# Kernel optimization log

Hardware: AMD Instinct MI355X
Metric: run time of the kernel (lower is better)

## Reference

```python
import jax, jax.numpy as jnp
import numpy as np

N, E, D, H = 50000, 1600000, 256, 256
EPS = 1e-5

def prelu(x, a):
    return jnp.where(x >= 0, x, a * x)

def batch_norm(x, gamma, beta):
    # training-mode BatchNorm1d: stats over the node (batch) dim
    mu = jnp.mean(x, axis=0)
    var = jnp.var(x, axis=0)
    return (x - mu) * jax.lax.rsqrt(var + EPS) * gamma + beta

def gcn_conv(x, edge_index, W, b):
    # PyG GCNConv: h = XW, add self-loops, symmetric norm, scatter-add, + bias
    h = x @ W
    n = x.shape[0]
    row = jnp.concatenate([edge_index[0], jnp.arange(n)])
    col = jnp.concatenate([edge_index[1], jnp.arange(n)])
    w = jnp.ones(row.shape[0], dtype=x.dtype)
    deg = jax.ops.segment_sum(w, col, num_segments=n)
    dinv = jnp.where(deg > 0, jax.lax.rsqrt(deg), 0.0)
    norm = dinv[row] * w * dinv[col]  # [E+N]
    msg = h[row] * norm[:, None]      # [E+N, H] gathered messages
    out = jax.ops.segment_sum(msg, col, num_segments=n)
    return out + b

def setup_inputs() -> dict:
    key = jax.random.key(0)
    ks = jax.random.split(key, 10)
    x = jax.random.normal(ks[0], (N, D), dtype=jnp.float32)
    edge_index = jax.random.randint(ks[1], (2, E), 0, N).astype(jnp.int64)
    s1 = 1.0 / np.sqrt(D)
    s2 = 1.0 / np.sqrt(H)
    return {
        "x": x,
        "edge_index": edge_index,
        "W1": jax.random.uniform(ks[2], (D, H), jnp.float32, -s1, s1),
        "b1": jnp.zeros((H,), jnp.float32),
        "W2": jax.random.uniform(ks[3], (H, H), jnp.float32, -s2, s2),
        "b2": jnp.zeros((H,), jnp.float32),
        "prelu_a": jnp.asarray(0.25, jnp.float32),
        "bn_gamma": jnp.ones((H,), jnp.float32),
        "bn_beta": jnp.zeros((H,), jnp.float32),
        "proj_W": jax.random.uniform(ks[4], (H, H), jnp.float32, -s2, s2),
        "proj_b": jnp.zeros((H,), jnp.float32),
        "pbn_gamma": jnp.ones((H,), jnp.float32),
        "pbn_beta": jnp.zeros((H,), jnp.float32),
        "prelu2_a": jnp.asarray(0.25, jnp.float32),
    }

def reference(x, edge_index, W1, b1, W2, b2, prelu_a, bn_gamma, bn_beta,
              proj_W, proj_b, pbn_gamma, pbn_beta, prelu2_a):
    # eval-mode dropout (identity); BN uses batch stats
    z = prelu(gcn_conv(x, edge_index, W1, b1), prelu_a)
    z = prelu(gcn_conv(z, edge_index, W2, b2), prelu_a)
    z = batch_norm(z, bn_gamma, bn_beta)
    p = prelu(batch_norm(z @ proj_W + proj_b, pbn_gamma, pbn_beta), prelu2_a)
    return (z, p)
```

## Files before the change

### kernel.cpp

```cpp
#include <hip/hip_runtime.h>
#include <hip/hip_bf16.h>


#define CAP 96
#define NPB 64
#define CHUNK 2048
#define SEGBIG 2432
#define MAXBKT 1024
#define SEGSTR 16

typedef __attribute__((ext_vector_type(8))) short short8;
typedef __attribute__((ext_vector_type(4))) float f32x4;

__device__ __forceinline__ float bf2f(unsigned short u) {
    union { unsigned int i; float f; } v; v.i = ((unsigned int)u) << 16; return v.f;
}
__device__ __forceinline__ unsigned short f2bf(float f) {
    __hip_bfloat16 h = __float2bfloat16(f);
    return *reinterpret_cast<unsigned short*>(&h);
}

__global__ __launch_bounds__(256) void k_zero(int* segcnt, int nbkt, float* stats) {
    int i = blockIdx.x * 256 + threadIdx.x;
    if (i < nbkt * SEGSTR) segcnt[i] = 0;
    if (i < 2048) stats[i] = 0.0f;
}

__global__ __launch_bounds__(64) void k_zrow(unsigned short* hs, int N) {
    ((ushort4*)hs)[(size_t)N * 64 + threadIdx.x] = ushort4{0, 0, 0, 0};
}

__global__ __launch_bounds__(256) void k_binh(const int* __restrict__ row, const int* __restrict__ col,
                                              unsigned* __restrict__ bins, int* __restrict__ segcnt,
                                              int E, int nbkt) {
    __shared__ int hist[MAXBKT];
    __shared__ int base[MAXBKT];
    int e0 = blockIdx.x * CHUNK;
    int eend = e0 + CHUNK; if (eend > E) eend = E;
    for (int b = threadIdx.x; b < nbkt; b += 256) hist[b] = 0;
    __syncthreads();
    for (int e = e0 + threadIdx.x; e < eend; e += 256)
        atomicAdd(&hist[col[e] >> 6], 1);
    __syncthreads();
    for (int b = threadIdx.x; b < nbkt; b += 256) {
        int h = hist[b];
        base[b] = h ? atomicAdd(&segcnt[b * SEGSTR], h) : 0;
        hist[b] = 0;
    }
    __syncthreads();
    for (int e = e0 + threadIdx.x; e < eend; e += 256) {
        int v = col[e], r = row[e];
        int b = v >> 6;
        int p = base[b] + atomicAdd(&hist[b], 1);
        if (p < SEGBIG) bins[(size_t)b * SEGBIG + p] = ((unsigned)r << 6) | (unsigned)(v & (NPB - 1));
    }
}

__global__ __launch_bounds__(256) void k_csr(const unsigned* __restrict__ bins, const int* __restrict__ segcnt,
                                             int* __restrict__ csr, int* __restrict__ fillp,
                                             float* __restrict__ dinv, int N) {
    __shared__ int cnt[NPB];
    int bkt = blockIdx.x;
    if (threadIdx.x < NPB) cnt[threadIdx.x] = 0;
    __syncthreads();
    int m = segcnt[bkt * SEGSTR]; if (m > SEGBIG) m = SEGBIG;
    const unsigned* b = bins + (size_t)bkt * SEGBIG;
    for (int i = threadIdx.x; i < m; i += 256) {
        unsigned ent = b[i];
        int loc = (int)(ent & (NPB - 1));
        int r   = (int)(ent >> 6);
        int p = atomicAdd(&cnt[loc], 1);
        if (p < CAP) csr[(size_t)(bkt * NPB + loc) * CAP + p] = r;
    }
    __syncthreads();
    if (threadIdx.x < NPB) {
        int v = bkt * NPB + threadIdx.x;
        if (v < N) {
            int c = cnt[threadIdx.x];
            int real = c < CAP ? c : CAP;
            int pc = (real + 15) & ~15;
            if (pc > CAP) pc = CAP;
            int* lst = csr + (size_t)v * CAP;
            for (int p = real; p < pc; ++p) lst[p] = N;
            fillp[v] = pc;
            dinv[v] = rsqrtf(1.0f + (float)c);
        }
    }
}

__global__ __launch_bounds__(256) void k_castx(const float* __restrict__ x, unsigned short* __restrict__ xb, size_t n4) {
    size_t stride = (size_t)gridDim.x * blockDim.x;
    for (size_t i = (size_t)blockIdx.x * blockDim.x + threadIdx.x; i < n4; i += stride) {
        float4 v = ((const float4*)x)[i];
        ushort4 o; o.x = f2bf(v.x); o.y = f2bf(v.y); o.z = f2bf(v.z); o.w = f2bf(v.w);
        ((ushort4*)xb)[i] = o;
    }
}

__global__ __launch_bounds__(256) void k_wt(const float* __restrict__ W, unsigned short* __restrict__ Wt,
                                            const float* __restrict__ scp) {
    __shared__ float t[32][33];
    int bx = blockIdx.x * 32, by = blockIdx.y * 32;
    int x = threadIdx.x & 31, y = threadIdx.x >> 5;
#pragma unroll
    for (int i = 0; i < 32; i += 8) {
        float s = scp ? scp[by + y + i] : 1.0f;
        t[y + i][x] = W[(size_t)(by + y + i) * 256 + bx + x] * s;
    }
    __syncthreads();
#pragma unroll
    for (int i = 0; i < 32; i += 8)
        Wt[(size_t)(bx + y + i) * 256 + by + x] = f2bf(t[x][y + i]);
}

__global__ __launch_bounds__(256) void k_tvec(const float* __restrict__ W, const float* __restrict__ sh,
                                              float* __restrict__ tvec) {
    int n = threadIdx.x;
    float s = 0.0f;
    for (int k = 0; k < 256; ++k) s += sh[k] * W[(size_t)k * 256 + n];
    tvec[n] = s;
}

__global__ __launch_bounds__(256) void k_gemm_bf16(const unsigned short* __restrict__ A,
                                                   const unsigned short* __restrict__ Bt,
                                                   unsigned short* __restrict__ C,
                                                   const float* __restrict__ dinv, int use_scale,
                                                   const float* __restrict__ tvec, int use_bias,
                                                   int M) {
    __shared__ unsigned short buf[16384];
    unsigned short* As = buf;
    unsigned short* Bs = buf + 8192;
    int tid  = threadIdx.x;
    int lane = tid & 63, wid = tid >> 6;
    int wr = wid >> 1, wc = wid & 1;
    int row0 = blockIdx.x * 128;
    int col0 = blockIdx.y * 128;

    f32x4 acc[4][4];
#pragma unroll
    for (int m = 0; m < 4; ++m)
#pragma unroll
        for (int n = 0; n < 4; ++n) acc[m][n] = f32x4{0.f, 0.f, 0.f, 0.f};

    int srow = lane >> 3;
    int sk   = (lane & 7) * 8;

    for (int k0 = 0; k0 < 256; k0 += 64) {
#pragma unroll
        for (int i = 0; i < 4; ++i) {
            int u = i * 4 + wid;
            int arow = row0 + u * 8 + srow;
            if (arow >= M) arow = M - 1;
            const unsigned short* ga = A  + (size_t)arow * 256 + k0 + sk;
            const unsigned short* gb = Bt + (size_t)(col0 + u * 8 + srow) * 256 + k0 + sk;
            __builtin_amdgcn_global_load_lds((const __attribute__((address_space(1))) void*)ga,
                (__attribute__((address_space(3))) void*)(As + u * 512), 16, 0, 0);
            __builtin_amdgcn_global_load_lds((const __attribute__((address_space(1))) void*)gb,
                (__attribute__((address_space(3))) void*)(Bs + u * 512), 16, 0, 0);
        }
        __syncthreads();
#pragma unroll
        for (int kk = 0; kk < 64; kk += 32) {
            short8 a[4], b[4];
#pragma unroll
            for (int m = 0; m < 4; ++m)
                a[m] = *(const short8*)(As + (wr * 64 + m * 16 + (lane & 15)) * 64 + kk + (lane >> 4) * 8);
#pragma unroll
            for (int n = 0; n < 4; ++n)
                b[n] = *(const short8*)(Bs + (wc * 64 + n * 16 + (lane & 15)) * 64 + kk + (lane >> 4) * 8);
#pragma unroll
            for (int m = 0; m < 4; ++m)
#pragma unroll
                for (int n = 0; n < 4; ++n)
                    acc[m][n] = __builtin_amdgcn_mfma_f32_16x16x32_bf16(a[m], b[n], acc[m][n], 0, 0, 0);
        }
        __syncthreads();
    }

    float tn[4] = {0.f, 0.f, 0.f, 0.f};
    if (use_bias) {
#pragma unroll
        for (int n = 0; n < 4; ++n) tn[n] = tvec[col0 + wc * 64 + n * 16 + (lane & 15)];
    }
#pragma unroll
    for (int m = 0; m < 4; ++m)
#pragma unroll
        for (int r = 0; r < 4; ++r) {
            int lr = wr * 64 + m * 16 + (lane >> 4) * 4 + r;
#pragma unroll
            for (int n = 0; n < 4; ++n)
                buf[lr * 128 + wc * 64 + n * 16 + (lane & 15)] = f2bf(acc[m][n][r] + tn[n]);
        }
    __syncthreads();
#pragma unroll
    for (int j = 0; j < 8; ++j) {
        int c = j * 256 + tid;
        int r = c >> 4, cc = c & 15;
        int grow = row0 + r;
        if (grow < M) {
            short8 v = *(const short8*)(buf + r * 128 + cc * 8);
            if (use_scale) {
                float d = dinv[grow];
                short8 o;
#pragma unroll
                for (int t = 0; t < 8; ++t)
                    o[t] = (short)f2bf(bf2f((unsigned short)v[t]) * d);
                v = o;
            }
            *(short8*)(C + (size_t)grow * 256 + col0 + cc * 8) = v;
        }
    }
}

__global__ __launch_bounds__(256) void k_agg_bf(const unsigned short* __restrict__ hs,
                                                unsigned short* __restrict__ outb,
                                                const float* __restrict__ dinv, const int* __restrict__ csr,
                                                const int* __restrict__ fillp, const float* __restrict__ bias,
                                                const float* __restrict__ aptr, int N) {
    int wv = threadIdx.x >> 6, lane = threadIdx.x & 63;
    int v = blockIdx.x * 4 + wv;
    if (v >= N) return;
    const ushort4* h4 = (const ushort4*)hs;
    float dv = dinv[v];
    ushort4 hv = h4[(size_t)v * 64 + lane];
    float s0 = bf2f(hv.x), s1 = bf2f(hv.y), s2 = bf2f(hv.z), s3 = bf2f(hv.w);
    int n = fillp[v];
    const int* lst = csr + (size_t)v * CAP;
    for (int i = 0; i < n; i += 16) {
        int u[16];
        ushort4 a[16];
#pragma unroll
        for (int t = 0; t < 16; ++t) u[t] = lst[i + t];
#pragma unroll
        for (int t = 0; t < 16; ++t) a[t] = h4[(size_t)u[t] * 64 + lane];
#pragma unroll
        for (int t = 0; t < 16; ++t) {
            s0 += bf2f(a[t].x); s1 += bf2f(a[t].y);
            s2 += bf2f(a[t].z); s3 += bf2f(a[t].w);
        }
    }
    float al = *aptr;
    float4 bb = *(const float4*)(bias + lane * 4);
    float o0 = dv * s0 + bb.x, o1 = dv * s1 + bb.y, o2 = dv * s2 + bb.z, o3 = dv * s3 + bb.w;
    o0 = o0 >= 0.f ? o0 : al * o0;
    o1 = o1 >= 0.f ? o1 : al * o1;
    o2 = o2 >= 0.f ? o2 : al * o2;
    o3 = o3 >= 0.f ? o3 : al * o3;
    ushort4 o; o.x = f2bf(o0); o.y = f2bf(o1); o.z = f2bf(o2); o.w = f2bf(o3);
    ((ushort4*)outb)[(size_t)v * 64 + lane] = o;
}

__global__ __launch_bounds__(256) void k_bnstats_v(const unsigned short* __restrict__ X, float* __restrict__ sums, int N) {
    int w = threadIdx.x >> 6, lane = threadIdx.x & 63;
    int c4 = lane * 4;
    float4 s = {0.f, 0.f, 0.f, 0.f}, q = {0.f, 0.f, 0.f, 0.f};
    int rstride = gridDim.x * 4;
    for (int r = blockIdx.x * 4 + w; r < N; r += rstride) {
        ushort4 x4 = ((const ushort4*)X)[(size_t)r * 64 + lane];
        float a = bf2f(x4.x), b = bf2f(x4.y), c = bf2f(x4.z), d = bf2f(x4.w);
        s.x += a; s.y += b; s.z += c; s.w += d;
        q.x += a * a; q.y += b * b; q.z += c * c; q.w += d * d;
    }
    atomicAdd(&sums[c4 + 0], s.x); atomicAdd(&sums[c4 + 1], s.y);
    atomicAdd(&sums[c4 + 2], s.z); atomicAdd(&sums[c4 + 3], s.w);
    atomicAdd(&sums[256 + c4 + 0], q.x); atomicAdd(&sums[256 + c4 + 1], q.y);
    atomicAdd(&sums[256 + c4 + 2], q.z); atomicAdd(&sums[256 + c4 + 3], q.w);
}

__global__ __launch_bounds__(256) void k_bnfinal(float* stats, const float* __restrict__ gamma,
                                                 const float* __restrict__ beta, float invN) {
    int c = threadIdx.x;
    float mu = stats[c] * invN;
    float var = stats[256 + c] * invN - mu * mu;
    float rstd = rsqrtf(var + 1e-5f);
    float sc = rstd * gamma[c];
    stats[512 + c] = sc;
    stats[768 + c] = beta[c] - mu * sc;
}

__global__ __launch_bounds__(256) void k_bnapply_z(const unsigned short* __restrict__ in,
                                                   float* __restrict__ zout,
                                                   const float* __restrict__ scale, const float* __restrict__ shift,
                                                   size_t n4) {
    size_t stride = (size_t)gridDim.x * blockDim.x;
    for (size_t i = (size_t)blockIdx.x * blockDim.x + threadIdx.x; i < n4; i += stride) {
        int c4 = (int)(i & 63) * 4;
        ushort4 x4 = ((const ushort4*)in)[i];
        float4 sc = *(const float4*)(scale + c4);
        float4 sh = *(const float4*)(shift + c4);
        float4 y;
        y.x = bf2f(x4.x) * sc.x + sh.x;
        y.y = bf2f(x4.y) * sc.y + sh.y;
        y.z = bf2f(x4.z) * sc.z + sh.z;
        y.w = bf2f(x4.w) * sc.w + sh.w;
        ((float4*)zout)[i] = y;
    }
}

__global__ __launch_bounds__(256) void k_bnapply_p(const unsigned short* __restrict__ in,
                                                   float* __restrict__ pout,
                                                   const float* __restrict__ scale, const float* __restrict__ shift,
                                                   const float* __restrict__ aptr, size_t n4) {
    size_t stride = (size_t)gridDim.x * blockDim.x;
    float a = *aptr;
    for (size_t i = (size_t)blockIdx.x * blockDim.x + threadIdx.x; i < n4; i += stride) {
        int c4 = (int)(i & 63) * 4;
        ushort4 x4 = ((const ushort4*)in)[i];
        float4 sc = *(const float4*)(scale + c4);
        float4 sh = *(const float4*)(shift + c4);
        float4 y;
        y.x = bf2f(x4.x) * sc.x + sh.x;
        y.y = bf2f(x4.y) * sc.y + sh.y;
        y.z = bf2f(x4.z) * sc.z + sh.z;
        y.w = bf2f(x4.w) * sc.w + sh.w;
        y.x = y.x >= 0.f ? y.x : a * y.x;
        y.y = y.y >= 0.f ? y.y : a * y.y;
        y.z = y.z >= 0.f ? y.z : a * y.z;
        y.w = y.w >= 0.f ? y.w : a * y.w;
        ((float4*)pout)[i] = y;
    }
}

extern "C" void kernel_launch(void* const* d_in, const int* in_sizes, int n_in,
                              void* d_out, int out_size, void* d_ws, size_t ws_size,
                              hipStream_t stream) {
    const float* x     = (const float*)d_in[0];
    const int*   ei    = (const int*)d_in[1];
    const float* W1    = (const float*)d_in[2];
    const float* b1    = (const float*)d_in[3];
    const float* W2    = (const float*)d_in[4];
    const float* b2    = (const float*)d_in[5];
    const float* aptr  = (const float*)d_in[6];
    const float* gamma = (const float*)d_in[7];
    const float* beta  = (const float*)d_in[8];
    const float* projW = (const float*)d_in[9];
    const float* pgamma = (const float*)d_in[11];
    const float* pbeta  = (const float*)d_in[12];
    const float* a2ptr  = (const float*)d_in[13];

    int N = in_sizes[0] / 256;
    int E = in_sizes[1] / 2;
    const int* row = ei;
    const int* col = ei + E;

    float* out  = (float*)d_out;
    float* zout = out;
    float* pout = out + (size_t)N * 256;

    int nbkt = (N + NPB - 1) / NPB;

    size_t rowsz = (size_t)(N + 1) * 256;
    unsigned short* B0 = (unsigned short*)d_ws;
    unsigned short* B1 = B0 + rowsz;
    unsigned short* B2 = B1 + rowsz;
    unsigned short* Wt = B2 + rowsz;
    float* dinv  = (float*)(Wt + 3 * 65536);
    int*   fillp = (int*)(dinv + N + 1);
    int*   csr   = fillp + N;
    float* stats = (float*)(csr + (size_t)N * CAP);
    float* tvec  = stats + 2048;
    int*   segcnt= (int*)(tvec + 256);
    unsigned* bins = (unsigned*)(segcnt + (size_t)nbkt * SEGSTR);

    int nb_binh = (E + CHUNK - 1) / CHUNK;
    dim3 ggrid((N + 127) / 128, 2);
    dim3 wgrid(8, 8);
    int  agrid = (N + 3) / 4;
    size_t n4 = (size_t)N * 64;

    k_zero <<<64, 256, 0, stream>>>(segcnt, nbkt, stats);
    k_zrow <<<1, 64, 0, stream>>>(B1, N);
    k_binh <<<nb_binh, 256, 0, stream>>>(row, col, bins, segcnt, E, nbkt);
    k_csr  <<<nbkt, 256, 0, stream>>>(bins, segcnt, csr, fillp, dinv, N);
    k_castx<<<2048, 256, 0, stream>>>(x, B0, n4);
    k_wt   <<<wgrid, 256, 0, stream>>>(W1, Wt,         nullptr);
    k_wt   <<<wgrid, 256, 0, stream>>>(W2, Wt + 65536, nullptr);

    k_gemm_bf16<<<ggrid, 256, 0, stream>>>(B0, Wt, B1, dinv, 1, nullptr, 0, N);
    k_agg_bf   <<<agrid, 256, 0, stream>>>(B1, B2, dinv, csr, fillp, b1, aptr, N);
    k_gemm_bf16<<<ggrid, 256, 0, stream>>>(B2, Wt + 65536, B1, dinv, 1, nullptr, 0, N);
    k_agg_bf   <<<agrid, 256, 0, stream>>>(B1, B0, dinv, csr, fillp, b2, aptr, N);
    k_bnstats_v<<<128, 256, 0, stream>>>(B0, stats, N);
    k_bnfinal  <<<1, 256, 0, stream>>>(stats, gamma, beta, 1.0f / (float)N);
    k_wt   <<<wgrid, 256, 0, stream>>>(projW, Wt + 131072, stats + 512);
    k_tvec <<<1, 256, 0, stream>>>(projW, stats + 768, tvec);
    k_gemm_bf16<<<ggrid, 256, 0, stream>>>(B0, Wt + 131072, B1, dinv, 0, tvec, 1, N);
    k_bnapply_z<<<2048, 256, 0, stream>>>(B0, zout, stats + 512, stats + 768, n4);
    k_bnstats_v<<<128, 256, 0, stream>>>(B1, stats + 1024, N);
    k_bnfinal  <<<1, 256, 0, stream>>>(stats + 1024, pgamma, pbeta, 1.0f / (float)N);
    k_bnapply_p<<<2048, 256, 0, stream>>>(B1, pout, stats + 1536, stats + 1792, a2ptr, n4);
}
```

Measured before the change: 721.8 us.

## Widen aggregation gathers to 16B, enlarge CSR buckets, parallelize tvec

The aggregation kernel now gives each node half a wavefront, with each lane loading 8 bf16 values (16 bytes) per neighbor row. That halves the number of gather instructions and puts two nodes in each wave. Rows past a node's list length are padded with the zero row. The CSR binning now uses 128-node buckets with larger chunks, and k_tvec is split across 256 blocks with a shuffle reduction instead of running as one serial block. Mixing two nodes in one wave can leave lanes idle when the neighbor counts differ, and the larger bins raise the chance of overflowing SEGBIG.

```diff
diff --git a/kernel.cpp b/kernel.cpp
--- a/kernel.cpp
+++ b/kernel.cpp
@@ -3,13 +3,14 @@
 
 
 #define CAP 96
-#define NPB 64
-#define CHUNK 2048
-#define SEGBIG 2432
-#define MAXBKT 1024
+#define NPB 128
+#define CHUNK 4096
+#define SEGBIG 4608
+#define MAXBKT 512
 #define SEGSTR 16
 
 typedef __attribute__((ext_vector_type(8))) short short8;
+typedef __attribute__((ext_vector_type(8))) unsigned short u16x8;
 typedef __attribute__((ext_vector_type(4))) float f32x4;
 
 __device__ __forceinline__ float bf2f(unsigned short u) {
@@ -40,7 +41,7 @@
     for (int b = threadIdx.x; b < nbkt; b += 256) hist[b] = 0;
     __syncthreads();
     for (int e = e0 + threadIdx.x; e < eend; e += 256)
-        atomicAdd(&hist[col[e] >> 6], 1);
+        atomicAdd(&hist[col[e] >> 7], 1);
     __syncthreads();
     for (int b = threadIdx.x; b < nbkt; b += 256) {
         int h = hist[b];
@@ -50,9 +51,9 @@
     __syncthreads();
     for (int e = e0 + threadIdx.x; e < eend; e += 256) {
         int v = col[e], r = row[e];
-        int b = v >> 6;
+        int b = v >> 7;
         int p = base[b] + atomicAdd(&hist[b], 1);
-        if (p < SEGBIG) bins[(size_t)b * SEGBIG + p] = ((unsigned)r << 6) | (unsigned)(v & (NPB - 1));
+        if (p < SEGBIG) bins[(size_t)b * SEGBIG + p] = ((unsigned)r << 7) | (unsigned)(v & (NPB - 1));
     }
 }
 
@@ -68,7 +69,7 @@
     for (int i = threadIdx.x; i < m; i += 256) {
         unsigned ent = b[i];
         int loc = (int)(ent & (NPB - 1));
-        int r   = (int)(ent >> 6);
+        int r   = (int)(ent >> 7);
         int p = atomicAdd(&cnt[loc], 1);
         if (p < CAP) csr[(size_t)(bkt * NPB + loc) * CAP + p] = r;
     }
@@ -113,12 +114,14 @@
         Wt[(size_t)(bx + y + i) * 256 + by + x] = f2bf(t[x][y + i]);
 }
 
-__global__ __launch_bounds__(256) void k_tvec(const float* __restrict__ W, const float* __restrict__ sh,
-                                              float* __restrict__ tvec) {
-    int n = threadIdx.x;
+__global__ __launch_bounds__(64) void k_tvec(const float* __restrict__ W, const float* __restrict__ sh,
+                                             float* __restrict__ tvec) {
+    int n = blockIdx.x, l = threadIdx.x;
     float s = 0.0f;
-    for (int k = 0; k < 256; ++k) s += sh[k] * W[(size_t)k * 256 + n];
-    tvec[n] = s;
+    for (int k = l; k < 256; k += 64) s += sh[k] * W[(size_t)k * 256 + n];
+#pragma unroll
+    for (int off = 32; off; off >>= 1) s += __shfl_down(s, off);
+    if (l == 0) tvec[n] = s;
 }
 
 __global__ __launch_bounds__(256) void k_gemm_bf16(const unsigned short* __restrict__ A,
@@ -218,36 +221,43 @@
                                                 const int* __restrict__ fillp, const float* __restrict__ bias,
                                                 const float* __restrict__ aptr, int N) {
     int wv = threadIdx.x >> 6, lane = threadIdx.x & 63;
-    int v = blockIdx.x * 4 + wv;
-    if (v >= N) return;
-    const ushort4* h4 = (const ushort4*)hs;
-    float dv = dinv[v];
-    ushort4 hv = h4[(size_t)v * 64 + lane];
-    float s0 = bf2f(hv.x), s1 = bf2f(hv.y), s2 = bf2f(hv.z), s3 = bf2f(hv.w);
-    int n = fillp[v];
-    const int* lst = csr + (size_t)v * CAP;
-    for (int i = 0; i < n; i += 16) {
+    int half = lane >> 5, hl = lane & 31;
+    int v = blockIdx.x * 8 + wv * 2 + half;
+    bool valid = v < N;
+    int vread = valid ? v : N;
+    const u16x8* h8 = (const u16x8*)hs;
+    u16x8 hv = h8[(size_t)vread * 32 + hl];
+    float s[8];
+#pragma unroll
+    for (int j = 0; j < 8; ++j) s[j] = bf2f((unsigned short)hv[j]);
+    int n = valid ? fillp[v] : 0;
+    const int* lst = csr + (size_t)(valid ? v : 0) * CAP;
+    int nmax = max(n, __shfl_xor(n, 32));
+    for (int i = 0; i < nmax; i += 16) {
         int u[16];
-        ushort4 a[16];
-#pragma unroll
-        for (int t = 0; t < 16; ++t) u[t] = lst[i + t];
-#pragma unroll
-        for (int t = 0; t < 16; ++t) a[t] = h4[(size_t)u[t] * 64 + lane];
-#pragma unroll
-        for (int t = 0; t < 16; ++t) {
-            s0 += bf2f(a[t].x); s1 += bf2f(a[t].y);
-            s2 += bf2f(a[t].z); s3 += bf2f(a[t].w);
-        }
-    }
+#pragma unroll
+        for (int t = 0; t < 16; ++t) u[t] = (i + t < n) ? lst[i + t] : N;
+        u16x8 a[16];
+#pragma unroll
+        for (int t = 0; t < 16; ++t) a[t] = h8[(size_t)u[t] * 32 + hl];
+#pragma unroll
+        for (int t = 0; t < 16; ++t)
+#pragma unroll
+            for (int j = 0; j < 8; ++j) s[j] += bf2f((unsigned short)a[t][j]);
+    }
+    float dv = valid ? dinv[v] : 0.0f;
     float al = *aptr;
-    float4 bb = *(const float4*)(bias + lane * 4);
-    float o0 = dv * s0 + bb.x, o1 = dv * s1 + bb.y, o2 = dv * s2 + bb.z, o3 = dv * s3 + bb.w;
-    o0 = o0 >= 0.f ? o0 : al * o0;
-    o1 = o1 >= 0.f ? o1 : al * o1;
-    o2 = o2 >= 0.f ? o2 : al * o2;
-    o3 = o3 >= 0.f ? o3 : al * o3;
-    ushort4 o; o.x = f2bf(o0); o.y = f2bf(o1); o.z = f2bf(o2); o.w = f2bf(o3);
-    ((ushort4*)outb)[(size_t)v * 64 + lane] = o;
+    float4 bb0 = *(const float4*)(bias + hl * 8);
+    float4 bb1 = *(const float4*)(bias + hl * 8 + 4);
+    float bbv[8] = {bb0.x, bb0.y, bb0.z, bb0.w, bb1.x, bb1.y, bb1.z, bb1.w};
+    u16x8 o;
+#pragma unroll
+    for (int j = 0; j < 8; ++j) {
+        float y = dv * s[j] + bbv[j];
+        y = y >= 0.f ? y : al * y;
+        o[j] = f2bf(y);
+    }
+    if (valid) ((u16x8*)outb)[(size_t)v * 32 + hl] = o;
 }
 
 __global__ __launch_bounds__(256) void k_bnstats_v(const unsigned short* __restrict__ X, float* __restrict__ sums, int N) {
@@ -365,10 +375,10 @@
     int nb_binh = (E + CHUNK - 1) / CHUNK;
     dim3 ggrid((N + 127) / 128, 2);
     dim3 wgrid(8, 8);
-    int  agrid = (N + 3) / 4;
+    int  agrid = (N + 7) / 8;
     size_t n4 = (size_t)N * 64;
 
-    k_zero <<<64, 256, 0, stream>>>(segcnt, nbkt, stats);
+    k_zero <<<32, 256, 0, stream>>>(segcnt, nbkt, stats);
     k_zrow <<<1, 64, 0, stream>>>(B1, N);
     k_binh <<<nb_binh, 256, 0, stream>>>(row, col, bins, segcnt, E, nbkt);
     k_csr  <<<nbkt, 256, 0, stream>>>(bins, segcnt, csr, fillp, dinv, N);
@@ -383,7 +393,7 @@
     k_bnstats_v<<<128, 256, 0, stream>>>(B0, stats, N);
     k_bnfinal  <<<1, 256, 0, stream>>>(stats, gamma, beta, 1.0f / (float)N);
     k_wt   <<<wgrid, 256, 0, stream>>>(projW, Wt + 131072, stats + 512);
-    k_tvec <<<1, 256, 0, stream>>>(projW, stats + 768, tvec);
+    k_tvec <<<256, 64, 0, stream>>>(projW, stats + 768, tvec);
     k_gemm_bf16<<<ggrid, 256, 0, stream>>>(B0, Wt + 131072, B1, dinv, 0, tvec, 1, N);
     k_bnapply_z<<<2048, 256, 0, stream>>>(B0, zout, stats + 512, stats + 768, n4);
     k_bnstats_v<<<128, 256, 0, stream>>>(B1, stats + 1024, N);
```

Result: faster. 692.1 us (-4.1%).
